# Optimization experiments

Measured on AMD Instinct MI355X. Metric: run time of the kernel, lower is better.

The kernel has to match this reference:

```python
import jax, jax.numpy as jnp
import numpy as np

B, S, D, H = 1, 4096, 1024, 16
HD = D // H  # 64

def _precompute_freqs_cis(dim, end, theta=10000.0):
    freqs = 1.0 / theta ** (jnp.arange(0, dim, 2, dtype=jnp.float32) / dim)
    t = jnp.arange(end, dtype=jnp.float32)
    freqs = jnp.outer(t, freqs)
    return jnp.cos(freqs), jnp.sin(freqs)

def setup_inputs() -> dict:
    key = jax.random.key(0)
    ks = jax.random.split(key, 5)
    cos, sin = _precompute_freqs_cis(HD, S)
    scale = 1.0 / np.sqrt(D)
    return {
        "hidden_states": jax.random.normal(ks[0], (B, S, D), dtype=jnp.float32),
        "cos": cos,
        "sin": sin,
        "attention_mask": jnp.ones((B, S), dtype=jnp.float32),
        "Wq": jax.random.normal(ks[1], (D, D), dtype=jnp.float32) * scale,
        "Wk": jax.random.normal(ks[2], (D, D), dtype=jnp.float32) * scale,
        "Wv": jax.random.normal(ks[3], (D, D), dtype=jnp.float32) * scale,
        "Wo": jax.random.normal(ks[4], (D, D), dtype=jnp.float32) * scale,
    }

def _rope(x, cos, sin):
    # x: [B,S,H,HD]; cos/sin: [S,HD//2] -> broadcast [1,S,1,HD//2]
    c = cos[None, :, None, :]
    s = sin[None, :, None, :]
    x1, x2 = jnp.split(x, 2, axis=-1)
    return jnp.concatenate([x1 * c - x2 * s, x2 * c + x1 * s], axis=-1)

def reference(hidden_states, cos, sin, attention_mask, Wq, Wk, Wv, Wo):
    b, s, d = hidden_states.shape
    h, hd = H, HD
    q = (hidden_states @ Wq.T).reshape(b, s, h, hd)
    k = (hidden_states @ Wk.T).reshape(b, s, h, hd)
    v = (hidden_states @ Wv.T).reshape(b, s, h, hd)
    q = _rope(q, cos, sin)
    k = _rope(k, cos, sin)
    scaling = hd ** (-0.5)
    # [B,H,S,S] scores (naive full-matrix attention, matching source)
    scores = jnp.einsum('bqhd,bkhd->bhqk', q, k) * scaling
    mask_add = (1.0 - attention_mask)[:, None, None, :] * (-10000.0)
    scores = scores + mask_add
    attn = jax.nn.softmax(scores.astype(jnp.float32), axis=-1).astype(q.dtype)
    out = jnp.einsum('bhqk,bkhd->bqhd', attn, v).reshape(b, s, d)
    return out @ Wo.T
```

## Files before the change

### kernel.cpp

```cpp
#include <hip/hip_runtime.h>
#include <stdint.h>

#define S_LEN   4096
#define D_MODEL 1024
#define N_HEADS 16
#define HEAD_DIM 64
#define LDP 72

typedef __attribute__((ext_vector_type(8))) short bf16x8;
typedef __attribute__((ext_vector_type(4))) float f32x4;
typedef __attribute__((ext_vector_type(4))) unsigned short u16x4;
typedef unsigned short ushort_t;

#define LOG2E 1.44269504088896340736f

__device__ __forceinline__ ushort_t f2bf(float f) {
    union { float f; uint32_t u; } v; v.f = f;
    uint32_t u = v.u;
    return (ushort_t)((u + 0x7fffu + ((u >> 16) & 1u)) >> 16);
}
__device__ __forceinline__ ushort_t f2bf_fast(float f) {
    union { float f; uint32_t u; } v; v.f = f;
    return (ushort_t)((v.u + 0x8000u) >> 16);
}
__device__ __forceinline__ float ex2(float x) {
#if __has_builtin(__builtin_amdgcn_exp2f)
    return __builtin_amdgcn_exp2f(x);
#else
    return exp2f(x);
#endif
}
__device__ __forceinline__ bf16x8 cvt8f(const float* __restrict__ p) {
    bf16x8 r;
#pragma unroll
    for (int j = 0; j < 8; j++) r[j] = (short)f2bf_fast(p[j]);
    return r;
}
__device__ __forceinline__ void gl_lds16(const ushort_t* g, ushort_t* l) {
    __builtin_amdgcn_global_load_lds(
        (const __attribute__((address_space(1))) void*)g,
        (__attribute__((address_space(3))) void*)l,
        16, 0, 0);
}

__global__ __launch_bounds__(256)
void qkv_kernel(const float* __restrict__ Xf,
                const float* __restrict__ Wqf, const float* __restrict__ Wkf,
                const float* __restrict__ Wvf,
                ushort_t* __restrict__ Qo, ushort_t* __restrict__ Ko,
                ushort_t* __restrict__ Vto,
                const float* __restrict__ cosF, const float* __restrict__ sinF)
{
    __shared__ __align__(16) ushort_t As[128 * 64];
    __shared__ __align__(16) ushort_t Bs[128 * 64];

    const int t     = threadIdx.x;
    const int mode  = blockIdx.x >> 3;
    const int mBase = blockIdx.y * 128;
    const int nBase = (blockIdx.x & 7) * 128;
    const int lane  = t & 63;
    const int wid   = t >> 6;
    const int quad  = lane >> 4;
    const int l15   = lane & 15;
    const int sw    = l15 & 7;
    const int wm    = (wid & 1) * 64;
    const int wn    = (wid >> 1) * 64;

    const float* Wf = (mode == 0) ? Wqf : (mode == 1) ? Wkf : Wvf;

    f32x4 acc[4][4];
#pragma unroll
    for (int i = 0; i < 4; i++)
#pragma unroll
        for (int j = 0; j < 4; j++) acc[i][j] = (f32x4)(0.0f);

    for (int k0 = 0; k0 < D_MODEL; k0 += 64) {
#pragma unroll
        for (int i = 0; i < 4; i++) {
            int e   = (i * 256 + t) * 8;
            int row = e >> 6;
            int c   = ((e >> 3) & 7) ^ (row & 7);
            *(bf16x8*)(&As[e]) = cvt8f(&Xf[(size_t)(mBase + row) * D_MODEL + k0 + c * 8]);
            *(bf16x8*)(&Bs[e]) = cvt8f(&Wf[(size_t)(nBase + row) * D_MODEL + k0 + c * 8]);
        }
        __syncthreads();
#pragma unroll
        for (int ks = 0; ks < 2; ks++) {
            bf16x8 a[4], b[4];
            const int cc = ((ks * 4 + quad) ^ sw) * 8;
#pragma unroll
            for (int mt = 0; mt < 4; mt++)
                a[mt] = *(const bf16x8*)(&As[((wm + mt * 16 + l15) << 6) + cc]);
#pragma unroll
            for (int nt = 0; nt < 4; nt++)
                b[nt] = *(const bf16x8*)(&Bs[((wn + nt * 16 + l15) << 6) + cc]);
#pragma unroll
            for (int mt = 0; mt < 4; mt++)
#pragma unroll
                for (int nt = 0; nt < 4; nt++)
                    acc[mt][nt] = __builtin_amdgcn_mfma_f32_16x16x32_bf16(a[mt], b[nt], acc[mt][nt], 0, 0, 0);
        }
        __syncthreads();
    }

    if (mode == 2) {
#pragma unroll
        for (int mt = 0; mt < 4; mt++) {
            int m0 = mBase + wm + mt * 16 + quad * 4;
#pragma unroll
            for (int nt = 0; nt < 4; nt++) {
                int n = nBase + wn + nt * 16 + l15;
                u16x4 pk;
#pragma unroll
                for (int r = 0; r < 4; r++) pk[r] = f2bf(acc[mt][nt][r]);
                *(u16x4*)(&Vto[(size_t)n * S_LEN + m0]) = pk;
            }
        }
    } else {
        ushort_t* outB = (mode == 0) ? Qo : Ko;
        const float sc = (mode == 0) ? (0.125f * LOG2E) : 1.0f;
        const int hcb = nBase + wn;
#pragma unroll
        for (int nt = 0; nt < 2; nt++) {
            int f = nt * 16 + l15;
#pragma unroll
            for (int mt = 0; mt < 4; mt++) {
                int m0 = mBase + wm + mt * 16 + quad * 4;
#pragma unroll
                for (int r = 0; r < 4; r++) {
                    int srow = m0 + r;
                    float c = cosF[srow * 32 + f];
                    float s = sinF[srow * 32 + f];
                    float x1 = acc[mt][nt][r];
                    float x2 = acc[mt][nt + 2][r];
                    outB[(size_t)srow * D_MODEL + hcb + f]      = f2bf((x1 * c - x2 * s) * sc);
                    outB[(size_t)srow * D_MODEL + hcb + 32 + f] = f2bf((x2 * c + x1 * s) * sc);
                }
            }
        }
    }
}

__global__ __launch_bounds__(256)
void oproj_kernel(const ushort_t* __restrict__ Ab, const float* __restrict__ Wf,
                  float* __restrict__ outF)
{
    __shared__ __align__(16) ushort_t As[64 * 64];
    __shared__ __align__(16) ushort_t Bs[128 * 64];

    const int t     = threadIdx.x;
    const int mBase = blockIdx.y * 64;
    const int nBase = blockIdx.x * 128;
    const int lane  = t & 63;
    const int wid   = t >> 6;
    const int quad  = lane >> 4;
    const int l15   = lane & 15;
    const int sw    = l15 & 7;
    const int wm    = (wid & 1) * 32;
    const int wn    = (wid >> 1) * 64;

    f32x4 acc[2][4];
#pragma unroll
    for (int i = 0; i < 2; i++)
#pragma unroll
        for (int j = 0; j < 4; j++) acc[i][j] = (f32x4)(0.0f);

    for (int k0 = 0; k0 < D_MODEL; k0 += 64) {
#pragma unroll
        for (int i = 0; i < 2; i++) {
            int e = (i * 256 + t) * 8;
            int row = e >> 6;
            int c = ((e >> 3) & 7) ^ (row & 7);
            gl_lds16(&Ab[(size_t)(mBase + row) * D_MODEL + k0 + c * 8], &As[e]);
        }
#pragma unroll
        for (int i = 0; i < 4; i++) {
            int e = (i * 256 + t) * 8;
            int row = e >> 6;
            int c = ((e >> 3) & 7) ^ (row & 7);
            *(bf16x8*)(&Bs[e]) = cvt8f(&Wf[(size_t)(nBase + row) * D_MODEL + k0 + c * 8]);
        }
        __syncthreads();
#pragma unroll
        for (int ks = 0; ks < 2; ks++) {
            bf16x8 a[2], b[4];
            const int cc = ((ks * 4 + quad) ^ sw) * 8;
#pragma unroll
            for (int mt = 0; mt < 2; mt++)
                a[mt] = *(const bf16x8*)(&As[((wm + mt * 16 + l15) << 6) + cc]);
#pragma unroll
            for (int nt = 0; nt < 4; nt++)
                b[nt] = *(const bf16x8*)(&Bs[((wn + nt * 16 + l15) << 6) + cc]);
#pragma unroll
            for (int mt = 0; mt < 2; mt++)
#pragma unroll
                for (int nt = 0; nt < 4; nt++)
                    acc[mt][nt] = __builtin_amdgcn_mfma_f32_16x16x32_bf16(a[mt], b[nt], acc[mt][nt], 0, 0, 0);
        }
        __syncthreads();
    }

#pragma unroll
    for (int mt = 0; mt < 2; mt++) {
        int m0 = mBase + wm + mt * 16 + quad * 4;
#pragma unroll
        for (int nt = 0; nt < 4; nt++) {
            int n = nBase + wn + nt * 16 + l15;
#pragma unroll
            for (int r = 0; r < 4; r++)
                outF[(size_t)(m0 + r) * D_MODEL + n] = acc[mt][nt][r];
        }
    }
}

__global__ __launch_bounds__(256)
void attn_kernel(const ushort_t* __restrict__ Q, const ushort_t* __restrict__ K,
                 const ushort_t* __restrict__ Vt, const float* __restrict__ mask,
                 ushort_t* __restrict__ out)
{
    __shared__ __align__(16) ushort_t Ks[2][64 * 64];
    __shared__ __align__(16) ushort_t Vs[2][64 * 64];
    __shared__ __align__(16) ushort_t Ps[128 * LDP];

    const int t    = threadIdx.x;
    const int h    = blockIdx.y;
    const int qt   = blockIdx.x;
    const int lane = t & 63;
    const int wid  = t >> 6;
    const int quad = lane >> 4;
    const int l15  = lane & 15;
    const int sw   = l15 & 7;
    const int wq   = wid * 32;

    bf16x8 aq[2][2];
#pragma unroll
    for (int mt = 0; mt < 2; mt++)
#pragma unroll
        for (int ks = 0; ks < 2; ks++)
            aq[mt][ks] = *(const bf16x8*)(&Q[(size_t)(qt * 128 + wq + mt * 16 + l15) * D_MODEL
                                            + h * HEAD_DIM + ks * 32 + quad * 8]);

    bf16x8 ones;
#pragma unroll
    for (int j = 0; j < 8; j++) ones[j] = (short)0x3F80;

    const int e0 = t * 8,   e1 = (256 + t) * 8;
    const int r0 = e0 >> 6, r1 = e1 >> 6;
    const int c0 = ((e0 >> 3) & 7) ^ (r0 & 7);
    const int c1 = ((e1 >> 3) & 7) ^ (r1 & 7);
    const int p0 = ((r0 & 15) << 2) | (r0 >> 4);
    const int p1 = ((r1 & 15) << 2) | (r1 >> 4);
    const ushort_t* kS0 = K  + (size_t)p0 * D_MODEL + h * HEAD_DIM + c0 * 8;
    const ushort_t* kS1 = K  + (size_t)p1 * D_MODEL + h * HEAD_DIM + c1 * 8;
    const ushort_t* vS0 = Vt + (size_t)(h * HEAD_DIM + r0) * S_LEN + c0 * 8;
    const ushort_t* vS1 = Vt + (size_t)(h * HEAD_DIM + r1) * S_LEN + c1 * 8;
    const float*    mP  = mask + (l15 << 2);

    ushort_t* psw0 = &Ps[(wq + quad * 4) * LDP + (l15 << 2)];
    ushort_t* psw1 = &Ps[(wq + 16 + quad * 4) * LDP + (l15 << 2)];

    f32x4 o_acc[2][4];
    f32x4 l_frag[2];
#pragma unroll
    for (int mt = 0; mt < 2; mt++) {
        l_frag[mt] = (f32x4)(0.0f);
#pragma unroll
        for (int nt = 0; nt < 4; nt++) o_acc[mt][nt] = (f32x4)(0.0f);
    }

    gl_lds16(kS0, &Ks[0][e0]);
    gl_lds16(kS1, &Ks[0][e1]);
    gl_lds16(vS0, &Vs[0][e0]);
    gl_lds16(vS1, &Vs[0][e1]);
    kS0 += 64 * D_MODEL; kS1 += 64 * D_MODEL; vS0 += 64; vS1 += 64;

    for (int kt = 0; kt < S_LEN / 64; kt++) {
        const int cur = kt & 1, nxt = cur ^ 1;
        __syncthreads();

        f32x4 mq = *(const f32x4*)(mP);
        mP += 64;

        if (kt < S_LEN / 64 - 1) {
            gl_lds16(kS0, &Ks[nxt][e0]);
            gl_lds16(kS1, &Ks[nxt][e1]);
            gl_lds16(vS0, &Vs[nxt][e0]);
            gl_lds16(vS1, &Vs[nxt][e1]);
        }
        kS0 += 64 * D_MODEL; kS1 += 64 * D_MODEL; vS0 += 64; vS1 += 64;

        f32x4 sacc[2][4];
#pragma unroll
        for (int mt = 0; mt < 2; mt++)
#pragma unroll
            for (int nt = 0; nt < 4; nt++)
                sacc[mt][nt] = (f32x4)(fmaf(mq[nt], 14426.9504f, -14446.9504f));
#pragma unroll
        for (int ks = 0; ks < 2; ks++) {
            bf16x8 bk[4];
            const int cc = ((ks * 4 + quad) ^ sw) * 8;
#pragma unroll
            for (int nt = 0; nt < 4; nt++)
                bk[nt] = *(const bf16x8*)(&Ks[cur][((nt * 16 + l15) << 6) + cc]);
#pragma unroll
            for (int mt = 0; mt < 2; mt++)
#pragma unroll
                for (int nt = 0; nt < 4; nt++)
                    sacc[mt][nt] = __builtin_amdgcn_mfma_f32_16x16x32_bf16(aq[mt][ks], bk[nt], sacc[mt][nt], 0, 0, 0);
        }

#pragma unroll
        for (int mt = 0; mt < 2; mt++) {
            ushort_t* psw = mt ? psw1 : psw0;
#pragma unroll
            for (int r = 0; r < 4; r++) {
                u16x4 pk;
                pk[0] = f2bf_fast(ex2(sacc[mt][0][r]));
                pk[1] = f2bf_fast(ex2(sacc[mt][1][r]));
                pk[2] = f2bf_fast(ex2(sacc[mt][2][r]));
                pk[3] = f2bf_fast(ex2(sacc[mt][3][r]));
                *(u16x4*)(&psw[r * LDP]) = pk;
            }
        }

#pragma unroll
        for (int ks = 0; ks < 2; ks++) {
            bf16x8 ap[2], bv[4];
#pragma unroll
            for (int mt = 0; mt < 2; mt++)
                ap[mt] = *(const bf16x8*)(&Ps[(wq + mt * 16 + l15) * LDP + ks * 32 + quad * 8]);
            const int cc = ((ks * 4 + quad) ^ sw) * 8;
#pragma unroll
            for (int nt = 0; nt < 4; nt++)
                bv[nt] = *(const bf16x8*)(&Vs[cur][((nt * 16 + l15) << 6) + cc]);
#pragma unroll
            for (int mt = 0; mt < 2; mt++) {
#pragma unroll
                for (int nt = 0; nt < 4; nt++)
                    o_acc[mt][nt] = __builtin_amdgcn_mfma_f32_16x16x32_bf16(ap[mt], bv[nt], o_acc[mt][nt], 0, 0, 0);
                l_frag[mt] = __builtin_amdgcn_mfma_f32_16x16x32_bf16(ap[mt], ones, l_frag[mt], 0, 0, 0);
            }
        }
    }

#pragma unroll
    for (int mt = 0; mt < 2; mt++) {
#pragma unroll
        for (int r = 0; r < 4; r++) {
            float inv = 1.0f / fmaxf(l_frag[mt][r], 1e-30f);
            int srow = qt * 128 + wq + mt * 16 + quad * 4 + r;
#pragma unroll
            for (int nt = 0; nt < 4; nt++) {
                int col = h * HEAD_DIM + nt * 16 + l15;
                out[(size_t)srow * D_MODEL + col] = f2bf(o_acc[mt][nt][r] * inv);
            }
        }
    }
}

extern "C" void kernel_launch(void* const* d_in, const int* in_sizes, int n_in,
                              void* d_out, int out_size, void* d_ws, size_t ws_size,
                              hipStream_t stream)
{
    (void)in_sizes; (void)n_in; (void)out_size; (void)ws_size;

    const float* X    = (const float*)d_in[0];
    const float* cosF = (const float*)d_in[1];
    const float* sinF = (const float*)d_in[2];
    const float* mask = (const float*)d_in[3];
    const float* Wq   = (const float*)d_in[4];
    const float* Wk   = (const float*)d_in[5];
    const float* Wv   = (const float*)d_in[6];
    const float* Wo   = (const float*)d_in[7];

    const size_t SD = (size_t)S_LEN * D_MODEL;

    ushort_t* ws  = (ushort_t*)d_ws;
    ushort_t* Qb  = ws;
    ushort_t* Kb  = ws + SD;
    ushort_t* Vtb = ws + 2 * SD;
    ushort_t* Ab  = ws + 3 * SD;
    float* outF   = (float*)d_out;

    dim3 gQKV(24, 32), gO(8, 64), gA(S_LEN / 128, N_HEADS), bb(256);

    qkv_kernel<<<gQKV, bb, 0, stream>>>(X, Wq, Wk, Wv, Qb, Kb, Vtb, cosF, sinF);
    attn_kernel<<<gA, bb, 0, stream>>>(Qb, Kb, Vtb, mask, Ab);
    oproj_kernel<<<gO, bb, 0, stream>>>(Ab, Wo, outF);
}
```

Measured before the change: 292.1 us.

## Pre-convert QKV inputs to bf16 and double-buffer LDS in both GEMMs

Adds a conversion kernel that turns X, Wq, Wk and Wv into bf16 once, placing them in the output buffer as scratch. The QKV GEMM then streams bf16 tiles straight into double-buffered LDS with global_load_lds, so fp32 conversion no longer sits in its inner loop and one barrier per iteration is dropped. The output-projection GEMM is also double-buffered: A tiles are prefetched and W tiles are loaded into registers for the next step while MFMAs run. The cost is an extra launch and extra memory traffic for the converted copies, twice the LDS per block, and reliance on the output buffer being free as scratch until oproj writes it.

```diff
diff --git a/kernel.cpp b/kernel.cpp
--- a/kernel.cpp
+++ b/kernel.cpp
@@ -36,6 +36,12 @@
     for (int j = 0; j < 8; j++) r[j] = (short)f2bf_fast(p[j]);
     return r;
 }
+__device__ __forceinline__ bf16x8 pack8(f32x4 a, f32x4 b) {
+    bf16x8 r;
+#pragma unroll
+    for (int j = 0; j < 4; j++) { r[j] = (short)f2bf_fast(a[j]); r[4 + j] = (short)f2bf_fast(b[j]); }
+    return r;
+}
 __device__ __forceinline__ void gl_lds16(const ushort_t* g, ushort_t* l) {
     __builtin_amdgcn_global_load_lds(
         (const __attribute__((address_space(1))) void*)g,
@@ -44,15 +50,31 @@
 }
 
 __global__ __launch_bounds__(256)
-void qkv_kernel(const float* __restrict__ Xf,
-                const float* __restrict__ Wqf, const float* __restrict__ Wkf,
-                const float* __restrict__ Wvf,
+void cvtall_kernel(const float* __restrict__ X,  const float* __restrict__ Wq,
+                   const float* __restrict__ Wk, const float* __restrict__ Wv,
+                   ushort_t* __restrict__ Xb,  ushort_t* __restrict__ Wqb,
+                   ushort_t* __restrict__ Wkb, ushort_t* __restrict__ Wvb)
+{
+    int b = blockIdx.x;
+    const float* src; ushort_t* dst; size_t off;
+    if (b < 2048)      { src = X;  dst = Xb;  off = (size_t)b * 2048; }
+    else if (b < 2560) { src = Wq; dst = Wqb; off = (size_t)(b - 2048) * 2048; }
+    else if (b < 3072) { src = Wk; dst = Wkb; off = (size_t)(b - 2560) * 2048; }
+    else               { src = Wv; dst = Wvb; off = (size_t)(b - 3072) * 2048; }
+    size_t i = off + (size_t)threadIdx.x * 8;
+    *(bf16x8*)(dst + i) = cvt8f(src + i);
+}
+
+__global__ __launch_bounds__(256)
+void qkv_kernel(const ushort_t* __restrict__ Xb,
+                const ushort_t* __restrict__ Wqb, const ushort_t* __restrict__ Wkb,
+                const ushort_t* __restrict__ Wvb,
                 ushort_t* __restrict__ Qo, ushort_t* __restrict__ Ko,
                 ushort_t* __restrict__ Vto,
                 const float* __restrict__ cosF, const float* __restrict__ sinF)
 {
-    __shared__ __align__(16) ushort_t As[128 * 64];
-    __shared__ __align__(16) ushort_t Bs[128 * 64];
+    __shared__ __align__(16) ushort_t As[2][128 * 64];
+    __shared__ __align__(16) ushort_t Bs[2][128 * 64];
 
     const int t     = threadIdx.x;
     const int mode  = blockIdx.x >> 3;
@@ -66,7 +88,19 @@
     const int wm    = (wid & 1) * 64;
     const int wn    = (wid >> 1) * 64;
 
-    const float* Wf = (mode == 0) ? Wqf : (mode == 1) ? Wkf : Wvf;
+    const ushort_t* Wb = (mode == 0) ? Wqb : (mode == 1) ? Wkb : Wvb;
+
+    int e[4];
+    const ushort_t* xS[4];
+    const ushort_t* wS[4];
+#pragma unroll
+    for (int i = 0; i < 4; i++) {
+        e[i] = (i * 256 + t) * 8;
+        int row = e[i] >> 6;
+        int c   = ((e[i] >> 3) & 7) ^ (row & 7);
+        xS[i] = Xb + (size_t)(mBase + row) * D_MODEL + c * 8;
+        wS[i] = Wb + (size_t)(nBase + row) * D_MODEL + c * 8;
+    }
 
     f32x4 acc[4][4];
 #pragma unroll
@@ -74,33 +108,42 @@
 #pragma unroll
         for (int j = 0; j < 4; j++) acc[i][j] = (f32x4)(0.0f);
 
-    for (int k0 = 0; k0 < D_MODEL; k0 += 64) {
-#pragma unroll
-        for (int i = 0; i < 4; i++) {
-            int e   = (i * 256 + t) * 8;
-            int row = e >> 6;
-            int c   = ((e >> 3) & 7) ^ (row & 7);
-            *(bf16x8*)(&As[e]) = cvt8f(&Xf[(size_t)(mBase + row) * D_MODEL + k0 + c * 8]);
-            *(bf16x8*)(&Bs[e]) = cvt8f(&Wf[(size_t)(nBase + row) * D_MODEL + k0 + c * 8]);
-        }
+#pragma unroll
+    for (int i = 0; i < 4; i++) {
+        gl_lds16(xS[i], &As[0][e[i]]);
+        gl_lds16(wS[i], &Bs[0][e[i]]);
+        xS[i] += 64; wS[i] += 64;
+    }
+
+    for (int kt = 0; kt < 16; kt++) {
+        const int cur = kt & 1, nxt = cur ^ 1;
         __syncthreads();
+
+        if (kt < 15) {
+#pragma unroll
+            for (int i = 0; i < 4; i++) {
+                gl_lds16(xS[i], &As[nxt][e[i]]);
+                gl_lds16(wS[i], &Bs[nxt][e[i]]);
+                xS[i] += 64; wS[i] += 64;
+            }
+        }
+
 #pragma unroll
         for (int ks = 0; ks < 2; ks++) {
             bf16x8 a[4], b[4];
             const int cc = ((ks * 4 + quad) ^ sw) * 8;
 #pragma unroll
             for (int mt = 0; mt < 4; mt++)
-                a[mt] = *(const bf16x8*)(&As[((wm + mt * 16 + l15) << 6) + cc]);
+                a[mt] = *(const bf16x8*)(&As[cur][((wm + mt * 16 + l15) << 6) + cc]);
 #pragma unroll
             for (int nt = 0; nt < 4; nt++)
-                b[nt] = *(const bf16x8*)(&Bs[((wn + nt * 16 + l15) << 6) + cc]);
+                b[nt] = *(const bf16x8*)(&Bs[cur][((wn + nt * 16 + l15) << 6) + cc]);
 #pragma unroll
             for (int mt = 0; mt < 4; mt++)
 #pragma unroll
                 for (int nt = 0; nt < 4; nt++)
                     acc[mt][nt] = __builtin_amdgcn_mfma_f32_16x16x32_bf16(a[mt], b[nt], acc[mt][nt], 0, 0, 0);
         }
-        __syncthreads();
     }
 
     if (mode == 2) {
@@ -145,8 +188,8 @@
 void oproj_kernel(const ushort_t* __restrict__ Ab, const float* __restrict__ Wf,
                   float* __restrict__ outF)
 {
-    __shared__ __align__(16) ushort_t As[64 * 64];
-    __shared__ __align__(16) ushort_t Bs[128 * 64];
+    __shared__ __align__(16) ushort_t As[2][64 * 64];
+    __shared__ __align__(16) ushort_t Bs[2][128 * 64];
 
     const int t     = threadIdx.x;
     const int mBase = blockIdx.y * 64;
@@ -159,45 +202,78 @@
     const int wm    = (wid & 1) * 32;
     const int wn    = (wid >> 1) * 64;
 
+    int eA[2], eB[4];
+    const ushort_t* aS[2];
+    const float*    wS[4];
+#pragma unroll
+    for (int i = 0; i < 2; i++) {
+        eA[i] = (i * 256 + t) * 8;
+        int row = eA[i] >> 6;
+        int c   = ((eA[i] >> 3) & 7) ^ (row & 7);
+        aS[i] = Ab + (size_t)(mBase + row) * D_MODEL + c * 8;
+    }
+#pragma unroll
+    for (int i = 0; i < 4; i++) {
+        eB[i] = (i * 256 + t) * 8;
+        int row = eB[i] >> 6;
+        int c   = ((eB[i] >> 3) & 7) ^ (row & 7);
+        wS[i] = Wf + (size_t)(nBase + row) * D_MODEL + c * 8;
+    }
+
     f32x4 acc[2][4];
 #pragma unroll
     for (int i = 0; i < 2; i++)
 #pragma unroll
         for (int j = 0; j < 4; j++) acc[i][j] = (f32x4)(0.0f);
 
-    for (int k0 = 0; k0 < D_MODEL; k0 += 64) {
-#pragma unroll
-        for (int i = 0; i < 2; i++) {
-            int e = (i * 256 + t) * 8;
-            int row = e >> 6;
-            int c = ((e >> 3) & 7) ^ (row & 7);
-            gl_lds16(&Ab[(size_t)(mBase + row) * D_MODEL + k0 + c * 8], &As[e]);
-        }
-#pragma unroll
-        for (int i = 0; i < 4; i++) {
-            int e = (i * 256 + t) * 8;
-            int row = e >> 6;
-            int c = ((e >> 3) & 7) ^ (row & 7);
-            *(bf16x8*)(&Bs[e]) = cvt8f(&Wf[(size_t)(nBase + row) * D_MODEL + k0 + c * 8]);
-        }
+#pragma unroll
+    for (int i = 0; i < 2; i++) { gl_lds16(aS[i], &As[0][eA[i]]); aS[i] += 64; }
+#pragma unroll
+    for (int i = 0; i < 4; i++) {
+        f32x4 w0 = *(const f32x4*)(wS[i]);
+        f32x4 w1 = *(const f32x4*)(wS[i] + 4);
+        *(bf16x8*)(&Bs[0][eB[i]]) = pack8(w0, w1);
+        wS[i] += 64;
+    }
+
+    for (int kt = 0; kt < 16; kt++) {
+        const int cur = kt & 1, nxt = cur ^ 1;
         __syncthreads();
+
+        f32x4 wr[4][2];
+        if (kt < 15) {
+#pragma unroll
+            for (int i = 0; i < 2; i++) { gl_lds16(aS[i], &As[nxt][eA[i]]); aS[i] += 64; }
+#pragma unroll
+            for (int i = 0; i < 4; i++) {
+                wr[i][0] = *(const f32x4*)(wS[i]);
+                wr[i][1] = *(const f32x4*)(wS[i] + 4);
+                wS[i] += 64;
+            }
+        }
+
 #pragma unroll
         for (int ks = 0; ks < 2; ks++) {
             bf16x8 a[2], b[4];
             const int cc = ((ks * 4 + quad) ^ sw) * 8;
 #pragma unroll
             for (int mt = 0; mt < 2; mt++)
-                a[mt] = *(const bf16x8*)(&As[((wm + mt * 16 + l15) << 6) + cc]);
+                a[mt] = *(const bf16x8*)(&As[cur][((wm + mt * 16 + l15) << 6) + cc]);
 #pragma unroll
             for (int nt = 0; nt < 4; nt++)
-                b[nt] = *(const bf16x8*)(&Bs[((wn + nt * 16 + l15) << 6) + cc]);
+                b[nt] = *(const bf16x8*)(&Bs[cur][((wn + nt * 16 + l15) << 6) + cc]);
 #pragma unroll
             for (int mt = 0; mt < 2; mt++)
 #pragma unroll
                 for (int nt = 0; nt < 4; nt++)
                     acc[mt][nt] = __builtin_amdgcn_mfma_f32_16x16x32_bf16(a[mt], b[nt], acc[mt][nt], 0, 0, 0);
         }
-        __syncthreads();
+
+        if (kt < 15) {
+#pragma unroll
+            for (int i = 0; i < 4; i++)
+                *(bf16x8*)(&Bs[nxt][eB[i]]) = pack8(wr[i][0], wr[i][1]);
+        }
     }
 
 #pragma unroll
@@ -374,17 +450,25 @@
     const float* Wo   = (const float*)d_in[7];
 
     const size_t SD = (size_t)S_LEN * D_MODEL;
+    const size_t WD = (size_t)D_MODEL * D_MODEL;
 
     ushort_t* ws  = (ushort_t*)d_ws;
     ushort_t* Qb  = ws;
     ushort_t* Kb  = ws + SD;
     ushort_t* Vtb = ws + 2 * SD;
     ushort_t* Ab  = ws + 3 * SD;
-    float* outF   = (float*)d_out;
+
+    float*    outF = (float*)d_out;
+    ushort_t* ob   = (ushort_t*)d_out;
+    ushort_t* Xb   = ob;
+    ushort_t* Wqb  = Xb + SD;
+    ushort_t* Wkb  = Wqb + WD;
+    ushort_t* Wvb  = Wkb + WD;
 
     dim3 gQKV(24, 32), gO(8, 64), gA(S_LEN / 128, N_HEADS), bb(256);
 
-    qkv_kernel<<<gQKV, bb, 0, stream>>>(X, Wq, Wk, Wv, Qb, Kb, Vtb, cosF, sinF);
+    cvtall_kernel<<<3584, bb, 0, stream>>>(X, Wq, Wk, Wv, Xb, Wqb, Wkb, Wvb);
+    qkv_kernel<<<gQKV, bb, 0, stream>>>(Xb, Wqb, Wkb, Wvb, Qb, Kb, Vtb, cosF, sinF);
     attn_kernel<<<gA, bb, 0, stream>>>(Qb, Kb, Vtb, mask, Ab);
     oproj_kernel<<<gO, bb, 0, stream>>>(Ab, Wo, outF);
 }
```

New measurement: 252.0 us (median of 2 runs). -13.7%, faster.
